# Optimization experiments

Hardware: AMD Instinct MI355X
Metric: run time of the kernel (lower is better)

Reference implementation:

```python
import jax, jax.numpy as jnp
import numpy as np

N = 20000
E = 80000
D = 1024


def setup_inputs() -> dict:
    key = jax.random.key(0)
    ks = jax.random.split(key, 12)
    s1 = 1.0 / np.sqrt(2 * D)
    s2 = 1.0 / np.sqrt(D)
    return {
        "x": jax.random.normal(ks[0], (N, D), dtype=jnp.float32),
        "edge_index": jax.random.randint(ks[1], (2, E), 0, N, dtype=jnp.int64),
        "edge_attr": jax.random.normal(ks[2], (E, D), dtype=jnp.float32),
        "W1a": jax.random.uniform(ks[3], (2 * D, D), jnp.float32, -s1, s1),
        "b1a": jax.random.uniform(ks[4], (D,), jnp.float32, -s1, s1),
        "W1b": jax.random.uniform(ks[5], (D, D), jnp.float32, -s2, s2),
        "b1b": jax.random.uniform(ks[6], (D,), jnp.float32, -s2, s2),
        "W2a": jax.random.uniform(ks[7], (2 * D, D), jnp.float32, -s1, s1),
        "b2a": jax.random.uniform(ks[8], (D,), jnp.float32, -s1, s1),
        "W2b": jax.random.uniform(ks[9], (D, D), jnp.float32, -s2, s2),
        "b2b": jax.random.uniform(ks[10], (D,), jnp.float32, -s2, s2),
    }


def reference(x, edge_index, edge_attr, W1a, b1a, W1b, b1b, W2a, b2a, W2b, b2b):
    row, col = edge_index[0], edge_index[1]
    # gather source node features, concat edge features: [E, 2D]
    h = jnp.concatenate([x[row], edge_attr], axis=1)
    # node_mlp_1: Lin(2D,D) -> ReLU -> Lin(D,D)
    h = jax.nn.relu(h @ W1a + b1a) @ W1b + b1b  # [E, D]
    # scatter_mean over destination nodes (dim_size = N); empty segments -> 0
    sums = jax.ops.segment_sum(h, col, num_segments=N)  # [N, D]
    counts = jax.ops.segment_sum(jnp.ones((h.shape[0], 1), h.dtype), col, num_segments=N)
    mean = sums / jnp.maximum(counts, 1.0)
    # (scatter_max is computed in the torch code but its result is unused)
    out = jnp.concatenate([x, mean], axis=1)  # [N, 2D]
    # node_mlp_2
    return jax.nn.relu(out @ W2a + b2a) @ W2b + b2b  # [N, D]
```

## Files before the change

kernel.cpp:

```cpp
#include <hip/hip_runtime.h>
#include <stdint.h>

#define NN 20000
#define NE 80000
#define DD 1024

typedef __bf16 bf16x8 __attribute__((ext_vector_type(8)));
typedef float f32x4 __attribute__((ext_vector_type(4)));
typedef unsigned short u16;
typedef unsigned int u32;

__device__ __forceinline__ float bf2f(u16 v) { return __uint_as_float(((u32)v) << 16); }
__device__ __forceinline__ u16 f2bf(float f) { return (u16)((__float_as_uint(f) + 0x8000u) >> 16); }

__device__ __forceinline__ void lds_dma16(const u16* g, u16* l) {
  __builtin_amdgcn_global_load_lds((const __attribute__((address_space(1))) u32*)g,
                                   (__attribute__((address_space(3))) u32*)l, 16, 0, 0);
}

__global__ void detect_stride_k(const int* __restrict__ ei, int* flag) {
  if (threadIdx.x == 0) {
    int nz = 0;
    for (int i = 1; i < 128; i += 2) nz |= ei[i];
    *flag = (nz == 0) ? 2 : 1;
  }
}

__global__ void transpose_cvt_k(const float* __restrict__ in, u16* __restrict__ out) {
  __shared__ float tile[32][33];
  int bx = blockIdx.x * 32, by = blockIdx.y * 32;
  int tx = threadIdx.x & 31, ty = threadIdx.x >> 5;
#pragma unroll
  for (int s = 0; s < 4; s++)
    tile[ty + s * 8][tx] = in[(size_t)(by + ty + s * 8) * DD + bx + tx];
  __syncthreads();
#pragma unroll
  for (int s = 0; s < 4; s++)
    out[(size_t)(bx + ty + s * 8) * DD + by + tx] = f2bf(tile[tx][ty + s * 8]);
}

__global__ void cvt_bf16_k(const float4* __restrict__ in, ushort4* __restrict__ out, int n4) {
  int i = blockIdx.x * 256 + threadIdx.x;
  if (i < n4) {
    float4 f = in[i];
    ushort4 o;
    o.x = f2bf(f.x); o.y = f2bf(f.y); o.z = f2bf(f.z); o.w = f2bf(f.w);
    out[i] = o;
  }
}

__global__ void count_edges_k(const int* __restrict__ ei, const int* __restrict__ sflag,
                              int* __restrict__ cnt) {
  int e = blockIdx.x * 256 + threadIdx.x;
  if (e < NE) {
    int s = *sflag;
    atomicAdd(&cnt[ei[(size_t)s * (NE + e)]], 1);
  }
}

__global__ __launch_bounds__(1024) void scan_k(const int* __restrict__ cnt,
                                               int* __restrict__ rowptr, int* __restrict__ ofs) {
  __shared__ int part[1024];
  int t = threadIdx.x;
  int base = t * 20;
  int loc[20];
  int s = 0;
#pragma unroll
  for (int i = 0; i < 20; i++) {
    int v = (base + i < NN) ? cnt[base + i] : 0;
    loc[i] = s; s += v;
  }
  part[t] = s;
  __syncthreads();
  for (int d = 1; d < 1024; d <<= 1) {
    int v = (t >= d) ? part[t - d] : 0;
    __syncthreads();
    part[t] += v;
    __syncthreads();
  }
  int excl = (t > 0) ? part[t - 1] : 0;
#pragma unroll
  for (int i = 0; i < 20; i++)
    if (base + i < NN) { rowptr[base + i] = excl + loc[i]; ofs[base + i] = excl + loc[i]; }
  if (t == 1023) rowptr[NN] = part[1023];
}

__global__ void scatter_k(const int* __restrict__ ei, const int* __restrict__ sflag,
                          int* __restrict__ ofs, int* __restrict__ perm) {
  int e = blockIdx.x * 256 + threadIdx.x;
  if (e < NE) {
    int s = *sflag;
    int c = ei[(size_t)s * (NE + e)];
    perm[atomicAdd(&ofs[c], 1)] = e;
  }
}

__global__ void seg_mean_k(const u16* __restrict__ h, const int* __restrict__ rowptr,
                           const int* __restrict__ perm, u16* __restrict__ sbar) {
  int n = blockIdx.x, t = threadIdx.x;
  int beg = rowptr[n], end = rowptr[n + 1];
  float a0 = 0, a1 = 0, a2 = 0, a3 = 0;
  for (int i = beg; i < end; i++) {
    int e = perm[i];
    ushort4 v = *(const ushort4*)(h + (size_t)e * DD + t * 4);
    a0 += bf2f(v.x); a1 += bf2f(v.y); a2 += bf2f(v.z); a3 += bf2f(v.w);
  }
  float inv = (end > beg) ? 1.0f / (float)(end - beg) : 0.0f;
  ushort4 o;
  o.x = f2bf(a0 * inv); o.y = f2bf(a1 * inv); o.z = f2bf(a2 * inv); o.w = f2bf(a3 * inv);
  *(ushort4*)(sbar + (size_t)n * DD + t * 4) = o;
}

template <int EPI, int NSRC>
__global__ __launch_bounds__(256) void gemm_k(
    const u16* __restrict__ A0, const u16* __restrict__ A1,
    const u16* __restrict__ B0, const u16* __restrict__ B1, int M,
    const float* __restrict__ bias, float* __restrict__ Cout, u16* __restrict__ Cbf,
    const u16* __restrict__ Pg, u16* __restrict__ Hout,
    const int* __restrict__ eidx, const int* __restrict__ sflag,
    const int* __restrict__ cnt) {
  __shared__ __align__(16) u16 As[128 * 32];
  __shared__ __align__(16) u16 Bs[128 * 32];

  const int tid = threadIdx.x;
  const int lane = tid & 63;
  const int wv = tid >> 6;
  const int wm = wv >> 1, wn = wv & 1;
  const int mblk = blockIdx.y, nblk = blockIdx.x;
  const int lrow = lane & 15, kq = lane >> 4;

  int ss = 1;
  if constexpr (EPI == 1) ss = *sflag;

  size_t a_goff[2], b_goff[2];
  u16 *a_lb[2], *b_lb[2];
#pragma unroll
  for (int r = 0; r < 2; r++) {
    int p = (wv * 2 + r) * 64 + lane;
    int row = p >> 2, c = p & 3;
    int kc = c ^ ((row >> 1) & 3);
    a_goff[r] = (size_t)min(mblk * 128 + row, M - 1) * DD + kc * 8;
    b_goff[r] = (size_t)(nblk * 128 + row) * DD + kc * 8;
    a_lb[r] = &As[(wv * 2 + r) * 512];
    b_lb[r] = &Bs[(wv * 2 + r) * 512];
  }

  int a_fo[4], b_fo[4];
#pragma unroll
  for (int i = 0; i < 4; i++) {
    int m = wm * 64 + i * 16 + lrow;
    a_fo[i] = (m * 4 + (kq ^ ((m >> 1) & 3))) * 8;
    int n = wn * 64 + i * 16 + lrow;
    b_fo[i] = (n * 4 + (kq ^ ((n >> 1) & 3))) * 8;
  }

  f32x4 acc[4][4] = {};

  for (int src = 0; src < NSRC; src++) {
    const u16* Ag = src ? A1 : A0;
    const u16* Bg = src ? B1 : B0;
    for (int kt = 0; kt < DD / 32; kt++) {
#pragma unroll
      for (int r = 0; r < 2; r++) {
        lds_dma16(Ag + a_goff[r] + (size_t)kt * 32, a_lb[r]);
        lds_dma16(Bg + b_goff[r] + (size_t)kt * 32, b_lb[r]);
      }
      __syncthreads();
      bf16x8 af[4], bf[4];
#pragma unroll
      for (int i = 0; i < 4; i++) {
        af[i] = *(const bf16x8*)&As[a_fo[i]];
        bf[i] = *(const bf16x8*)&Bs[b_fo[i]];
      }
#pragma unroll
      for (int i = 0; i < 4; i++)
#pragma unroll
        for (int j = 0; j < 4; j++)
          acc[i][j] = __builtin_amdgcn_mfma_f32_16x16x32_bf16(af[i], bf[j], acc[i][j], 0, 0, 0);
      __syncthreads();
    }
  }

#pragma unroll
  for (int i = 0; i < 4; i++) {
#pragma unroll
    for (int r = 0; r < 4; r++) {
      int grow = mblk * 128 + wm * 64 + i * 16 + kq * 4 + r;
      if (grow >= M) continue;
      int erow = 0;
      if constexpr (EPI == 1) erow = eidx[(size_t)ss * grow];
#pragma unroll
      for (int j = 0; j < 4; j++) {
        int gcol = nblk * 128 + wn * 64 + j * 16 + lrow;
        float v = acc[i][j][r];
        if constexpr (EPI == 0) {
          Cout[(size_t)grow * DD + gcol] = v + bias[gcol];
        } else if constexpr (EPI == 1) {
          float z = fmaxf(v + bf2f(Pg[(size_t)erow * DD + gcol]), 0.0f);
          Hout[(size_t)grow * DD + gcol] = f2bf(z);
        } else if constexpr (EPI == 2) {
          float b = (cnt[grow] > 0) ? bias[gcol] : 0.0f;
          Cbf[(size_t)grow * DD + gcol] = f2bf(v + b);
        } else if constexpr (EPI == 3) {
          Cbf[(size_t)grow * DD + gcol] = f2bf(fmaxf(v + bias[gcol], 0.0f));
        } else {
          Cbf[(size_t)grow * DD + gcol] = f2bf(v + bias[gcol]);
        }
      }
    }
  }
}

extern "C" void kernel_launch(void* const* d_in, const int* in_sizes, int n_in,
                              void* d_out, int out_size, void* d_ws, size_t ws_size,
                              hipStream_t stream) {
  const float* x   = (const float*)d_in[0];
  const int*   ei  = (const int*)d_in[1];
  const float* ea  = (const float*)d_in[2];
  const float* W1a = (const float*)d_in[3];
  const float* b1a = (const float*)d_in[4];
  const float* W1b = (const float*)d_in[5];
  const float* b1b = (const float*)d_in[6];
  const float* W2a = (const float*)d_in[7];
  const float* b2a = (const float*)d_in[8];
  const float* W2b = (const float*)d_in[9];
  const float* b2b = (const float*)d_in[10];
  float* out = (float*)d_out;

  char* ws = (char*)d_ws;
  size_t off = 0;
  const size_t WSZ = (size_t)DD * DD;
  u16* W1aT_t = (u16*)(ws + off); off += WSZ * 2;
  u16* W1aT_b = (u16*)(ws + off); off += WSZ * 2;
  u16* W1bT   = (u16*)(ws + off); off += WSZ * 2;
  u16* W2aT_t = (u16*)(ws + off); off += WSZ * 2;
  u16* W2aT_b = (u16*)(ws + off); off += WSZ * 2;
  u16* W2bT   = (u16*)(ws + off); off += WSZ * 2;
  u16* xb   = (u16*)(ws + off); off += (size_t)NN * DD * 2;
  u16* eb   = (u16*)(ws + off); off += (size_t)NE * DD * 2;
  u16* bufP = (u16*)(ws + off); off += (size_t)NN * DD * 2;
  u16* bufM = (u16*)(ws + off); off += (size_t)NN * DD * 2;
  u16* h    = (u16*)(ws + off); off += (size_t)NE * DD * 2;
  int* cnt    = (int*)(ws + off); off += (size_t)NN * 4;
  int* rowptr = (int*)(ws + off); off += (size_t)(NN + 1) * 4;
  int* ofs    = (int*)(ws + off); off += (size_t)NN * 4;
  int* perm   = (int*)(ws + off); off += (size_t)NE * 4;
  int* sflag  = (int*)(ws + off); off += 256;
  if (ws_size < off) return;

  dim3 tb(256);
  dim3 tg(32, 32);
  transpose_cvt_k<<<tg, tb, 0, stream>>>(W1a, W1aT_t);
  transpose_cvt_k<<<tg, tb, 0, stream>>>(W1a + WSZ, W1aT_b);
  transpose_cvt_k<<<tg, tb, 0, stream>>>(W1b, W1bT);
  transpose_cvt_k<<<tg, tb, 0, stream>>>(W2a, W2aT_t);
  transpose_cvt_k<<<tg, tb, 0, stream>>>(W2a + WSZ, W2aT_b);
  transpose_cvt_k<<<tg, tb, 0, stream>>>(W2b, W2bT);

  cvt_bf16_k<<<NN * DD / 4 / 256, tb, 0, stream>>>((const float4*)x, (ushort4*)xb, NN * DD / 4);
  cvt_bf16_k<<<NE * DD / 4 / 256, tb, 0, stream>>>((const float4*)ea, (ushort4*)eb, NE * DD / 4);

  detect_stride_k<<<1, 64, 0, stream>>>(ei, sflag);
  hipMemsetAsync(cnt, 0, (size_t)NN * 4, stream);
  count_edges_k<<<(NE + 255) / 256, tb, 0, stream>>>(ei, sflag, cnt);
  scan_k<<<1, 1024, 0, stream>>>(cnt, rowptr, ofs);
  scatter_k<<<(NE + 255) / 256, tb, 0, stream>>>(ei, sflag, ofs, perm);

  dim3 gN(8, (NN + 127) / 128);
  dim3 gE(8, NE / 128);

  gemm_k<4, 1><<<gN, tb, 0, stream>>>(xb, nullptr, W1aT_t, nullptr, NN,
                                      b1a, nullptr, bufP, nullptr, nullptr,
                                      nullptr, nullptr, nullptr);
  gemm_k<1, 1><<<gE, tb, 0, stream>>>(eb, nullptr, W1aT_b, nullptr, NE,
                                      nullptr, nullptr, nullptr, bufP, h,
                                      ei, sflag, nullptr);
  seg_mean_k<<<NN, tb, 0, stream>>>(h, rowptr, perm, bufP);
  gemm_k<2, 1><<<gN, tb, 0, stream>>>(bufP, nullptr, W1bT, nullptr, NN,
                                      b1b, nullptr, bufM, nullptr, nullptr,
                                      nullptr, nullptr, cnt);
  gemm_k<3, 2><<<gN, tb, 0, stream>>>(xb, bufM, W2aT_t, W2aT_b, NN,
                                      b2a, nullptr, bufP, nullptr, nullptr,
                                      nullptr, nullptr, nullptr);
  gemm_k<0, 1><<<gN, tb, 0, stream>>>(bufP, nullptr, W2bT, nullptr, NN,
                                      b2b, out, nullptr, nullptr, nullptr,
                                      nullptr, nullptr, nullptr);
}
```

Before: 1.320 ms.

## Double-buffer GEMM LDS tiles and remap block IDs for XCD-local L2 reuse

The GEMM kernel now keeps two LDS buffers for the A and B tiles. It issues the global-to-LDS DMA for the next K-step before running the MFMAs on the current one, which cuts the barriers per step from two to one and overlaps load latency with compute. The 2D grid is flattened to 1D and remapped so that blocks landing on the same XCD (bid mod 8) cover the same M row-block across all 8 N-blocks, which should improve L2 reuse of A. The cost is twice the LDS per block, which may lower occupancy.

```diff
diff --git a/kernel.cpp b/kernel.cpp
--- a/kernel.cpp
+++ b/kernel.cpp
@@ -119,21 +119,27 @@
     const u16* __restrict__ Pg, u16* __restrict__ Hout,
     const int* __restrict__ eidx, const int* __restrict__ sflag,
     const int* __restrict__ cnt) {
-  __shared__ __align__(16) u16 As[128 * 32];
-  __shared__ __align__(16) u16 Bs[128 * 32];
+  __shared__ __align__(16) u16 As[2][128 * 32];
+  __shared__ __align__(16) u16 Bs[2][128 * 32];
 
   const int tid = threadIdx.x;
   const int lane = tid & 63;
   const int wv = tid >> 6;
   const int wm = wv >> 1, wn = wv & 1;
-  const int mblk = blockIdx.y, nblk = blockIdx.x;
+
+  const int nwg = gridDim.x;
+  const int cpx = nwg >> 3;
+  const int bid = blockIdx.x;
+  const int l = (bid & 7) * cpx + (bid >> 3);
+  const int nblk = l & 7, mblk = l >> 3;
+
   const int lrow = lane & 15, kq = lane >> 4;
 
   int ss = 1;
   if constexpr (EPI == 1) ss = *sflag;
 
   size_t a_goff[2], b_goff[2];
-  u16 *a_lb[2], *b_lb[2];
+  int lseg[2];
 #pragma unroll
   for (int r = 0; r < 2; r++) {
     int p = (wv * 2 + r) * 64 + lane;
@@ -141,8 +147,7 @@
     int kc = c ^ ((row >> 1) & 3);
     a_goff[r] = (size_t)min(mblk * 128 + row, M - 1) * DD + kc * 8;
     b_goff[r] = (size_t)(nblk * 128 + row) * DD + kc * 8;
-    a_lb[r] = &As[(wv * 2 + r) * 512];
-    b_lb[r] = &Bs[(wv * 2 + r) * 512];
+    lseg[r] = (wv * 2 + r) * 512;
   }
 
   int a_fo[4], b_fo[4];
@@ -156,29 +161,41 @@
 
   f32x4 acc[4][4] = {};
 
-  for (int src = 0; src < NSRC; src++) {
-    const u16* Ag = src ? A1 : A0;
-    const u16* Bg = src ? B1 : B0;
-    for (int kt = 0; kt < DD / 32; kt++) {
-#pragma unroll
-      for (int r = 0; r < 2; r++) {
-        lds_dma16(Ag + a_goff[r] + (size_t)kt * 32, a_lb[r]);
-        lds_dma16(Bg + b_goff[r] + (size_t)kt * 32, b_lb[r]);
-      }
-      __syncthreads();
-      bf16x8 af[4], bf[4];
-#pragma unroll
-      for (int i = 0; i < 4; i++) {
-        af[i] = *(const bf16x8*)&As[a_fo[i]];
-        bf[i] = *(const bf16x8*)&Bs[b_fo[i]];
-      }
-#pragma unroll
-      for (int i = 0; i < 4; i++)
-#pragma unroll
-        for (int j = 0; j < 4; j++)
-          acc[i][j] = __builtin_amdgcn_mfma_f32_16x16x32_bf16(af[i], bf[j], acc[i][j], 0, 0, 0);
-      __syncthreads();
+  const int NK = NSRC * (DD / 32);
+
+  auto stage = [&](int b, int step) {
+    const u16* Ag = A0;
+    const u16* Bg = B0;
+    if constexpr (NSRC == 2) {
+      if (step >= DD / 32) { Ag = A1; Bg = B1; }
     }
+    size_t ko = (size_t)(step & (DD / 32 - 1)) * 32;
+#pragma unroll
+    for (int r = 0; r < 2; r++) {
+      lds_dma16(Ag + a_goff[r] + ko, &As[b][lseg[r]]);
+      lds_dma16(Bg + b_goff[r] + ko, &Bs[b][lseg[r]]);
+    }
+  };
+
+  stage(0, 0);
+  __syncthreads();
+
+  int cur = 0;
+  for (int step = 0; step < NK; step++) {
+    if (step + 1 < NK) stage(cur ^ 1, step + 1);
+    bf16x8 af[4], bf[4];
+#pragma unroll
+    for (int i = 0; i < 4; i++) {
+      af[i] = *(const bf16x8*)&As[cur][a_fo[i]];
+      bf[i] = *(const bf16x8*)&Bs[cur][b_fo[i]];
+    }
+#pragma unroll
+    for (int i = 0; i < 4; i++)
+#pragma unroll
+      for (int j = 0; j < 4; j++)
+        acc[i][j] = __builtin_amdgcn_mfma_f32_16x16x32_bf16(af[i], bf[j], acc[i][j], 0, 0, 0);
+    __syncthreads();
+    cur ^= 1;
   }
 
 #pragma unroll
@@ -266,8 +283,10 @@
   scan_k<<<1, 1024, 0, stream>>>(cnt, rowptr, ofs);
   scatter_k<<<(NE + 255) / 256, tb, 0, stream>>>(ei, sflag, ofs, perm);
 
-  dim3 gN(8, (NN + 127) / 128);
-  dim3 gE(8, NE / 128);
+  const int nmbN = (NN + 127) / 128;
+  const int nmbE = NE / 128;
+  dim3 gN(8 * nmbN);
+  dim3 gE(8 * nmbE);
 
   gemm_k<4, 1><<<gN, tb, 0, stream>>>(xb, nullptr, W1aT_t, nullptr, NN,
                                       b1a, nullptr, bufP, nullptr, nullptr,
```

New measurement: 1.275 ms. -3.5%, faster.
